# Optimization experiments

Hardware: AMD Instinct MI355X
Metric: run time of the kernel (lower is better)

Reference implementation:

```python
import jax, jax.numpy as jnp
import numpy as np

N, CIN, T, V = 32, 64, 256, 25
COUT = 192
K = 3                      # num_subset
INTER = COUT // 4          # coff_embedding = 4 -> 48
MID = COUT // 3            # 64
EPS = 1e-5


def _bn(x, g, b):
    # training-mode BatchNorm2d over (N, T, V) per channel
    m = x.mean(axis=(0, 2, 3), keepdims=True)
    v = x.var(axis=(0, 2, 3), keepdims=True)
    return (x - m) * jax.lax.rsqrt(v + EPS) * g[None, :, None, None] + b[None, :, None, None]


def _conv1x1(x, w, b):
    # w: [O, C]
    return jnp.einsum('oc,nctv->notv', w, x) + b[None, :, None, None]


def _tconv(x, w, b, pad):
    # w: [O, C, k, 1] temporal conv along T
    y = jax.lax.conv_general_dilated(x, w, (1, 1), ((pad, pad), (0, 0)),
                                     dimension_numbers=('NCHW', 'OIHW', 'NCHW'))
    return y + b[None, :, None, None]


def setup_inputs() -> dict:
    key = jax.random.key(0)
    ks = jax.random.split(key, 24)
    r = lambda i, shape, s=0.05: jax.random.normal(ks[i], shape, jnp.float32) * s
    return {
        'x': r(0, (N, CIN, T, V), 1.0),
        'A': jax.random.uniform(ks[1], (K, V, V), jnp.float32),   # fixed adjacency buffer
        'PA': jnp.full((K, V, V), 1e-6, jnp.float32),
        'Wa': r(2, (K, INTER, CIN)), 'ba': jnp.zeros((K, INTER), jnp.float32),
        'Wb': r(3, (K, INTER, CIN)), 'bb': jnp.zeros((K, INTER), jnp.float32),
        'Wd': r(4, (K, COUT, CIN)), 'bd': jnp.zeros((K, COUT), jnp.float32),
        'gcn_bn_g': jnp.ones(COUT, jnp.float32), 'gcn_bn_b': jnp.zeros(COUT, jnp.float32),
        'down_w': r(5, (COUT, CIN)), 'down_b': jnp.zeros(COUT, jnp.float32),
        'down_bn_g': jnp.ones(COUT, jnp.float32), 'down_bn_b': jnp.zeros(COUT, jnp.float32),
        'W11': r(6, (COUT, COUT)), 'b11': jnp.zeros(COUT, jnp.float32),
        'W21': r(7, (COUT, COUT)), 'b21': jnp.zeros(COUT, jnp.float32),
        'W31': r(8, (COUT, COUT)), 'b31': jnp.zeros(COUT, jnp.float32),
        'W12': r(9, (MID, COUT, 1, 1)), 'b12': jnp.zeros(MID, jnp.float32),
        'W22': r(10, (MID, COUT, 3, 1)), 'b22': jnp.zeros(MID, jnp.float32),
        'W32': r(11, (MID, COUT, 7, 1)), 'b32': jnp.zeros(MID, jnp.float32),
        'tcn_bn_g': jnp.ones(COUT, jnp.float32), 'tcn_bn_b': jnp.zeros(COUT, jnp.float32),
        'res_w': r(12, (COUT, CIN)), 'res_b': jnp.zeros(COUT, jnp.float32),
        'res_bn_g': jnp.ones(COUT, jnp.float32), 'res_bn_b': jnp.zeros(COUT, jnp.float32),
    }


def reference(x, A, PA, Wa, ba, Wb, bb, Wd, bd, gcn_bn_g, gcn_bn_b,
              down_w, down_b, down_bn_g, down_bn_b,
              W11, b11, W21, b21, W31, b31, W12, b12, W22, b22, W32, b32,
              tcn_bn_g, tcn_bn_b, res_w, res_b, res_bn_g, res_bn_b):
    n, c, t, v = x.shape
    # ---- unit_gcn (all num_subset branches vectorized over axis k) ----
    fa = jnp.einsum('kic,nctv->nkitv', Wa, x) + ba[None, :, :, None, None]
    fb = jnp.einsum('kic,nctv->nkitv', Wb, x) + bb[None, :, :, None, None]
    A1 = fa.transpose(0, 1, 4, 2, 3).reshape(n, K, v, INTER * t)   # [n,k,V,inter*T]
    A2 = fb.reshape(n, K, INTER * t, v)                            # [n,k,inter*T,V]
    scores = jnp.einsum('nkvd,nkdw->nkvw', A1, A2) / A1.shape[-1]
    att = jax.nn.softmax(scores, axis=-2) + (A + PA)[None]         # softmax over rows (dim -2)
    xv = x.reshape(n, c * t, v)
    z = jnp.einsum('ndv,nkvw->nkdw', xv, att).reshape(n, K, c, t, v)
    y = jnp.einsum('koc,nkctv->notv', Wd, z) + bd.sum(axis=0)[None, :, None, None]
    y = _bn(y, gcn_bn_g, gcn_bn_b)
    y = y + _bn(_conv1x1(x, down_w, down_b), down_bn_g, down_bn_b)
    g = jax.nn.relu(y)
    # ---- unit_tcn_m: three parallel (1x1 conv -> temporal conv) branches ----
    x1 = _tconv(_conv1x1(g, W11, b11), W12, b12, 0)
    x2 = _tconv(_conv1x1(g, W21, b21), W22, b22, 1)
    x3 = _tconv(_conv1x1(g, W31, b31), W32, b32, 3)
    tm = _bn(jnp.concatenate([x1, x2, x3], axis=1), tcn_bn_g, tcn_bn_b)
    # ---- residual: 1x1 unit_tcn on original input ----
    res = _bn(_conv1x1(x, res_w, res_b), res_bn_g, res_bn_b)
    return jax.nn.relu(tm + res)
```

## Files before the change

kernel.cpp:

```cpp
#include <hip/hip_runtime.h>
#include <hip/hip_bf16.h>
#include <cstdint>
#include <cstddef>

#define EPS_  1e-5f
#define NTV_  204800

typedef unsigned short u16;
typedef __attribute__((ext_vector_type(8))) short short8;
typedef __attribute__((ext_vector_type(4))) float f32x4;

__device__ __forceinline__ float bf2f(u16 u) {
  uint32_t x = (uint32_t)u << 16;
  float f;
  __builtin_memcpy(&f, &x, 4);
  return f;
}
__device__ __forceinline__ u16 f2bf(float f) {
  uint32_t x;
  __builtin_memcpy(&x, &f, 4);
  uint32_t r = (x + 0x7FFFu + ((x >> 16) & 1u)) >> 16;
  return (u16)r;
}

__device__ __forceinline__ void gload_lds16(const u16* g, u16* l) {
  __builtin_amdgcn_global_load_lds(
      (const __attribute__((address_space(1))) uint32_t*)g,
      (__attribute__((address_space(3))) uint32_t*)l, 16, 0, 0);
}

__global__ __launch_bounds__(256) void k_cvtw(
    const float* __restrict__ Wa, const float* __restrict__ Wb_,
    const float* __restrict__ dw, const float* __restrict__ rw,
    const float* __restrict__ W11, const float* __restrict__ W21, const float* __restrict__ W31,
    const float* __restrict__ Wd, const float* __restrict__ W12, const float* __restrict__ W22,
    const float* __restrict__ W32, const float* __restrict__ bd,
    const float* __restrict__ ba, const float* __restrict__ bb,
    const float* __restrict__ downbi, const float* __restrict__ resbi,
    const float* __restrict__ b11, const float* __restrict__ b21, const float* __restrict__ b31,
    u16* __restrict__ WB, float* __restrict__ bd2, float* __restrict__ fbias,
    float* __restrict__ cbias)
{
  int i = blockIdx.x * 256 + threadIdx.x;
  if (i < 9216) { WB[i] = f2bf(Wa[i]); return; }
  i -= 9216;
  if (i < 9216) { WB[9216 + i] = f2bf(Wb_[i]); return; }
  i -= 9216;
  if (i < 12288) { WB[18432 + i] = f2bf(dw[i]); return; }
  i -= 12288;
  if (i < 12288) { WB[30720 + i] = f2bf(rw[i]); return; }
  i -= 12288;
  if (i < 36864) { WB[43008 + i] = f2bf(W11[i]); return; }
  i -= 36864;
  if (i < 36864) { WB[79872 + i] = f2bf(W21[i]); return; }
  i -= 36864;
  if (i < 36864) { WB[116736 + i] = f2bf(W31[i]); return; }
  i -= 36864;
  if (i < 36864) {
    const int o = i / 192, r = i % 192, k = r >> 6, c = r & 63;
    WB[153600 + i] = f2bf(Wd[((size_t)(k * 192 + o)) * 64 + c]);
    return;
  }
  i -= 36864;
  if (i < 12288) { WB[190464 + i] = f2bf(W12[i]); return; }
  i -= 12288;
  if (i < 36864) {
    const int tap = i / 12288, q = i % 12288, o = q / 192, c = q % 192;
    WB[202752 + i] = f2bf(W22[((size_t)(o * 192 + c)) * 3 + tap]);
    return;
  }
  i -= 36864;
  if (i < 86016) {
    const int tap = i / 12288, q = i % 12288, o = q / 192, c = q % 192;
    WB[239616 + i] = f2bf(W32[((size_t)(o * 192 + c)) * 7 + tap]);
    return;
  }
  i -= 86016;
  if (i < 192) { bd2[i] = bd[i] + bd[192 + i] + bd[384 + i]; return; }
  i -= 192;
  if (i < 288) { fbias[i] = (i < 144) ? ba[i] : bb[i - 144]; return; }
  i -= 288;
  if (i < 960) {
    const int g = i / 192, o = i % 192;
    float v;
    if (g == 0) v = downbi[o];
    else if (g == 1) v = resbi[o];
    else if (g == 2) v = b11[o];
    else if (g == 3) v = b21[o];
    else v = b31[o];
    cbias[i] = v;
  }
}

__global__ __launch_bounds__(256) void k_xpose(const float* __restrict__ x, u16* __restrict__ xb)
{
  __shared__ u16 xt[256][72];
  const int bx = blockIdx.x;
  const int n = bx / 25, s0 = (bx % 25) * 256;
  const int tid = threadIdx.x;
  for (int l = tid; l < 64 * 64; l += 256) {
    const int c = l >> 6, q = l & 63;
    float4 v = *(const float4*)&x[((size_t)n * 64 + c) * 6400 + s0 + q * 4];
    xt[q * 4 + 0][c] = f2bf(v.x);
    xt[q * 4 + 1][c] = f2bf(v.y);
    xt[q * 4 + 2][c] = f2bf(v.z);
    xt[q * 4 + 3][c] = f2bf(v.w);
  }
  __syncthreads();
  for (int l = tid; l < 256 * 8; l += 256) {
    const int row = l >> 3, seg = l & 7;
    const int s_old = s0 + row;
    const int dv = s_old % 25, dt = s_old / 25;
    *(uint4*)&xb[((size_t)n * 6400 + dv * 256 + dt) * 64 + seg * 8] = *(const uint4*)&xt[row][seg * 8];
  }
}

template<int C, int NP, bool STATS>
__global__ __launch_bounds__(256, 2) void k_conv4(
    const u16* __restrict__ in, const u16* __restrict__ Wb,
    const float* __restrict__ bias,
    u16* __restrict__ out0, u16* __restrict__ out1, u16* __restrict__ out2,
    float* __restrict__ stSum, float* __restrict__ stSq)
{
  constexpr int CS = C / 8;
  constexpr int CH = C / 32;
  __shared__ u16 Bt[128 * C];
  __shared__ u16 Ep[4][16 * 24];

  const int bx = blockIdx.x;
  const int nb = bx / 50;
  const int sb = (bx % 50) * 128;
  const int tid = threadIdx.x;
  const int w = tid >> 6, lane = tid & 63;
  const int lr = lane & 15, lg = lane >> 4;

  constexpr int SB = 128 * CS;
#pragma unroll
  for (int base = 0; base < SB; base += 256) {
    const int slot = base + tid;
    const int r = slot / CS, q = slot % CS;
    gload_lds16(&in[((size_t)nb * 6400 + sb + r) * C + ((q ^ (r & 7)) << 3)],
                &Bt[(size_t)(base + w * 64) * 8]);
  }
  __syncthreads();

  const int row2 = lane >> 2, q2 = lane & 3;

  for (int p = 0; p < NP; ++p) {
    u16* outp = (p == 0) ? out0 : ((p == 1) ? out1 : out2);
    const u16* Ap = Wb + (size_t)p * 192 * C;
    short8 af[3][CH];
#pragma unroll
    for (int mi = 0; mi < 3; ++mi)
#pragma unroll
      for (int j = 0; j < CH; ++j)
        af[mi][j] = *(const short8*)&Ap[((size_t)(w * 48 + mi * 16 + lr)) * C + j * 32 + lg * 8];
    float4 bv[3];
#pragma unroll
    for (int mi = 0; mi < 3; ++mi)
      bv[mi] = *(const float4*)&bias[p * 192 + w * 48 + mi * 16 + lg * 4];
    float ssum[3][4] = {}, ssq[3][4] = {};

#pragma unroll
    for (int t = 0; t < 8; ++t) {
      f32x4 acc[3];
#pragma unroll
      for (int mi = 0; mi < 3; ++mi) {
        acc[mi][0] = 0.f; acc[mi][1] = 0.f; acc[mi][2] = 0.f; acc[mi][3] = 0.f;
      }
      const int rr = t * 16 + lr;
#pragma unroll
      for (int j = 0; j < CH; ++j) {
        short8 bf = *(const short8*)&Bt[((size_t)rr * CS + ((j * 4 + lg) ^ (rr & 7))) * 8];
#pragma unroll
        for (int mi = 0; mi < 3; ++mi)
          acc[mi] = __builtin_amdgcn_mfma_f32_16x16x32_bf16(af[mi][j], bf, acc[mi], 0, 0, 0);
      }
#pragma unroll
      for (int mi = 0; mi < 3; ++mi) {
        u16* sc = Ep[w];
#pragma unroll
        for (int r = 0; r < 4; ++r) {
          float vv = acc[mi][r] + ((const float*)&bv[mi])[r];
          if (STATS) { ssum[mi][r] += vv; ssq[mi][r] += vv * vv; }
          sc[lr * 24 + lg * 4 + r] = f2bf(vv);
        }
        uint2 val = *(const uint2*)&sc[row2 * 24 + q2 * 4];
        *(uint2*)&outp[((size_t)nb * 6400 + sb + t * 16 + row2) * 192 +
                       w * 48 + mi * 16 + q2 * 4] = val;
      }
    }

    if (STATS) {
#pragma unroll
      for (int mi = 0; mi < 3; ++mi)
#pragma unroll
        for (int r = 0; r < 4; ++r) {
          float ss = ssum[mi][r], sq = ssq[mi][r];
#pragma unroll
          for (int m = 1; m < 16; m <<= 1) { ss += __shfl_xor(ss, m); sq += __shfl_xor(sq, m); }
          if (lr == 0) {
            const int og = p * 192 + w * 48 + mi * 16 + lg * 4 + r;
            const int slot = bx & 15;
            atomicAdd(&stSum[og * 16 + slot], ss);
            atomicAdd(&stSq[og * 16 + slot], sq);
          }
        }
    }
  }
}

template<int KT>
__global__ __launch_bounds__(256, 2) void k_tconv4(
    const u16* __restrict__ in, const u16* __restrict__ Wb,
    const float* __restrict__ bias, u16* __restrict__ out,
    float* __restrict__ stSum, float* __restrict__ stSq,
    const u16* __restrict__ zp, int o_off)
{
  constexpr int C = 192, CS = 24, CH = 6;
  constexpr int HALO = KT / 2;
  constexpr int BR = 128 + 2 * HALO;
  __shared__ u16 Bt[BR * C];
  __shared__ u16 Ep[4][16 * 24];

  const int bx = blockIdx.x;
  const int nb = bx / 50;
  const int sb = (bx % 50) * 128;
  const int tbase = sb & 255;
  const int tid = threadIdx.x;
  const int w = tid >> 6, lane = tid & 63;
  const int lr = lane & 15, lg = lane >> 4;

  constexpr int SB = BR * CS;
  for (int base = 0; base < SB; base += 256) {
    const int slot = base + tid;
    if ((SB % 256 == 0) || slot < SB) {
      const int r = slot / CS, q = slot % CS;
      const int t = tbase - HALO + r;
      const u16* src = (HALO == 0 || (unsigned)t < 256u)
          ? &in[((size_t)nb * 6400 + sb - HALO + r) * C + ((q ^ (r & 7)) << 3)]
          : zp;
      gload_lds16(src, &Bt[(size_t)(base + w * 64) * 8]);
    }
  }
  __syncthreads();

  f32x4 acc[8];
#pragma unroll
  for (int t = 0; t < 8; ++t) {
    acc[t][0] = 0.f; acc[t][1] = 0.f; acc[t][2] = 0.f; acc[t][3] = 0.f;
  }

  for (int tap = 0; tap < KT; ++tap) {
    short8 af[CH];
#pragma unroll
    for (int j = 0; j < CH; ++j)
      af[j] = *(const short8*)&Wb[((size_t)(tap * 64 + w * 16 + lr)) * C + j * 32 + lg * 8];
#pragma unroll
    for (int t = 0; t < 8; ++t) {
      const int rr = t * 16 + lr + tap;
#pragma unroll
      for (int j = 0; j < CH; ++j) {
        short8 bf = *(const short8*)&Bt[((size_t)rr * CS + ((j * 4 + lg) ^ (rr & 7))) * 8];
        acc[t] = __builtin_amdgcn_mfma_f32_16x16x32_bf16(af[j], bf, acc[t], 0, 0, 0);
      }
    }
  }

  const float4 bv4 = *(const float4*)&bias[w * 16 + lg * 4];
  const int row2 = lane >> 2, q2 = lane & 3;
  float ssum[4] = {}, ssq[4] = {};
#pragma unroll
  for (int t = 0; t < 8; ++t) {
    u16* sc = Ep[w];
#pragma unroll
    for (int r = 0; r < 4; ++r) {
      float vv = acc[t][r] + ((const float*)&bv4)[r];
      ssum[r] += vv; ssq[r] += vv * vv;
      sc[lr * 24 + lg * 4 + r] = f2bf(vv);
    }
    uint2 val = *(const uint2*)&sc[row2 * 24 + q2 * 4];
    *(uint2*)&out[((size_t)nb * 6400 + sb + t * 16 + row2) * 192 +
                  o_off + w * 16 + q2 * 4] = val;
  }
#pragma unroll
  for (int r = 0; r < 4; ++r) {
    float ss = ssum[r], sq = ssq[r];
#pragma unroll
    for (int m = 1; m < 16; m <<= 1) { ss += __shfl_xor(ss, m); sq += __shfl_xor(sq, m); }
    if (lr == 0) {
      const int og = o_off + w * 16 + lg * 4 + r;
      const int slot = bx & 15;
      atomicAdd(&stSum[og * 16 + slot], ss);
      atomicAdd(&stSq[og * 16 + slot], sq);
    }
  }
}

__global__ __launch_bounds__(256) void k_gemm_cf(
    const u16* __restrict__ in, const u16* __restrict__ Wb,
    const float* __restrict__ bias, u16* __restrict__ out)
{
  __shared__ u16 Bt[128 * 64];
  __shared__ u16 At[288 * 64];
  __shared__ u16 SC[48 * 136];

  const int bx = blockIdx.x;
  const int nb = bx / 50;
  const int sb = (bx % 50) * 128;
  const int v = sb >> 8, tbase = sb & 255;
  const int tid = threadIdx.x;
  const int w = tid >> 6, lane = tid & 63;
  const int lr = lane & 15, lg = lane >> 4;
  const int s_w = w * 32;

  for (int base = 0; base < 1024; base += 256) {
    const int slot = base + tid;
    const int r = slot >> 3, q = slot & 7;
    gload_lds16(&in[((size_t)nb * 6400 + v * 256 + tbase + r) * 64 + ((q ^ (r & 7)) << 3)],
                &Bt[(size_t)(base + w * 64) * 8]);
  }
  for (int base = 0; base < 2304; base += 256) {
    const int slot = base + tid;
    const int r = slot >> 3, q = slot & 7;
    gload_lds16(&Wb[(size_t)r * 64 + ((q ^ (r & 7)) << 3)],
                &At[(size_t)(base + w * 64) * 8]);
  }
  __syncthreads();

  for (int p = 0; p < 6; ++p) {
    f32x4 acc[3][2];
#pragma unroll
    for (int mi = 0; mi < 3; ++mi)
#pragma unroll
      for (int ni = 0; ni < 2; ++ni) {
        acc[mi][ni][0] = 0.f; acc[mi][ni][1] = 0.f; acc[mi][ni][2] = 0.f; acc[mi][ni][3] = 0.f;
      }
#pragma unroll
    for (int ch = 0; ch < 2; ++ch) {
      const int j = ch * 4 + lg;
      short8 af[3], bf[2];
#pragma unroll
      for (int mi = 0; mi < 3; ++mi) {
        const int r = p * 48 + mi * 16 + lr;
        af[mi] = *(const short8*)&At[((size_t)r * 8 + (j ^ (r & 7))) * 8];
      }
#pragma unroll
      for (int ni = 0; ni < 2; ++ni) {
        const int r = s_w + ni * 16 + lr;
        bf[ni] = *(const short8*)&Bt[((size_t)r * 8 + (j ^ (r & 7))) * 8];
      }
#pragma unroll
      for (int mi = 0; mi < 3; ++mi)
#pragma unroll
        for (int ni = 0; ni < 2; ++ni)
          acc[mi][ni] = __builtin_amdgcn_mfma_f32_16x16x32_bf16(af[mi], bf[ni], acc[mi][ni], 0, 0, 0);
    }
#pragma unroll
    for (int mi = 0; mi < 3; ++mi)
#pragma unroll
      for (int r = 0; r < 4; ++r) {
        const float bv = bias[p * 48 + mi * 16 + lg * 4 + r];
#pragma unroll
        for (int ni = 0; ni < 2; ++ni) acc[mi][ni][r] += bv;
      }
    __syncthreads();
#pragma unroll
    for (int mi = 0; mi < 3; ++mi)
#pragma unroll
      for (int ni = 0; ni < 2; ++ni)
#pragma unroll
        for (int r = 0; r < 4; ++r)
          SC[(mi * 16 + lg * 4 + r) * 136 + s_w + ni * 16 + lr] = f2bf(acc[mi][ni][r]);
    __syncthreads();
#pragma unroll
    for (int it = 0; it < 3; ++it) {
      const int row = it * 16 + (tid >> 4), chunk = tid & 15;
      *(uint4*)&out[((size_t)nb * 288 + p * 48 + row) * 6400 + sb + chunk * 8] =
          *(const uint4*)&SC[row * 136 + chunk * 8];
    }
  }
}

__device__ __forceinline__ float dot4(uint2 a, uint2 b) {
  return bf2f((u16)(a.x & 0xffff)) * bf2f((u16)(b.x & 0xffff)) +
         bf2f((u16)(a.x >> 16))    * bf2f((u16)(b.x >> 16)) +
         bf2f((u16)(a.y & 0xffff)) * bf2f((u16)(b.y & 0xffff)) +
         bf2f((u16)(a.y >> 16))    * bf2f((u16)(b.y >> 16));
}

__global__ __launch_bounds__(256) void k_scores_part(
    const u16* __restrict__ fab, float* __restrict__ part)
{
  const int nk = blockIdx.x;
  const int seg = blockIdx.y;
  const int n = nk / 3, k = nk % 3;
  __shared__ u16 sa[12800], sb[12800];
  const int tid = threadIdx.x;
  const u16* fap = fab + ((size_t)(n * 288 + k * 48 + seg * 2)) * 6400;
  const u16* fbp = fab + ((size_t)(n * 288 + 144 + k * 48 + seg * 2)) * 6400;
  for (int l = tid; l < 1600; l += 256) {
    ((uint4*)sa)[l] = ((const uint4*)fap)[l];
    ((uint4*)sb)[l] = ((const uint4*)fbp)[l];
  }
  __syncthreads();

  const int l0 = tid, l1 = tid + 256, l2 = tid + 512;
  const bool ok2 = (l2 < 625);
  const int v0 = l0 / 25, w0 = l0 % 25;
  const int v1 = l1 / 25, w1 = l1 % 25;
  const int v2 = ok2 ? l2 / 25 : 0, w2 = ok2 ? l2 % 25 : 0;
  float a0 = 0.f, a1 = 0.f, a2 = 0.f;
  const int rot = ((tid & 63) * 4) & 255;

#pragma unroll
  for (int ch = 0; ch < 2; ++ch) {
    const u16* pa = sa + ch * 6400;
    const u16* pb = sb + ch * 6400;
    for (int it = 0; it < 64; ++it) {
      const int t = (it * 4 + rot) & 255;
      a0 += dot4(*(const uint2*)&pa[v0 * 256 + t], *(const uint2*)&pb[w0 * 256 + t]);
      a1 += dot4(*(const uint2*)&pa[v1 * 256 + t], *(const uint2*)&pb[w1 * 256 + t]);
      if (ok2)
        a2 += dot4(*(const uint2*)&pa[v2 * 256 + t], *(const uint2*)&pb[w2 * 256 + t]);
    }
  }
  float* po = part + ((size_t)nk * 24 + seg) * 640;
  po[l0] = a0;
  po[l1] = a1;
  if (ok2) po[l2] = a2;
}

__global__ __launch_bounds__(256) void k_softmax(
    const float* __restrict__ part, const float* __restrict__ A,
    const float* __restrict__ PA, float* __restrict__ att)
{
  const int nk = blockIdx.x;
  const int n = nk / 3, k = nk % 3;
  __shared__ float sc[640];
  const int tid = threadIdx.x;
  const float* pb = part + (size_t)nk * 24 * 640;
  for (int l = tid; l < 625; l += 256) {
    float s = 0.f;
#pragma unroll
    for (int seg = 0; seg < 24; ++seg) s += pb[seg * 640 + l];
    sc[l] = s;
  }
  __syncthreads();
  if (tid < 25) {
    const int w = tid;
    const float scale = 1.f / 12288.f;
    float m = -1e30f;
    for (int v = 0; v < 25; ++v) m = fmaxf(m, sc[v * 25 + w]);
    m *= scale;
    float e[25], sum = 0.f;
#pragma unroll
    for (int v = 0; v < 25; ++v) { e[v] = __expf(sc[v * 25 + w] * scale - m); sum += e[v]; }
    const float inv = 1.f / sum;
    const float* Ak = A + k * 625;
    const float* Pk = PA + k * 625;
    float* ao = att + ((size_t)n * 3 + k) * 625;
#pragma unroll
    for (int v = 0; v < 25; ++v) ao[v * 25 + w] = e[v] * inv + Ak[v * 25 + w] + Pk[v * 25 + w];
  }
}

__global__ __launch_bounds__(256) void k_z(
    const u16* __restrict__ xb, const float* __restrict__ att, u16* __restrict__ z)
{
  __shared__ float attl[1950];
  __shared__ u16 xt[12800];
  const int bx = blockIdx.x;
  const int n = bx >> 5, tb = (bx & 31) * 8;
  const int tid = threadIdx.x;

  for (int l = tid; l < 1875; l += 256) {
    const int k = l / 625, vw = l % 625, v = vw / 25, w = vw % 25;
    attl[(k * 25 + v) * 26 + w] = att[((size_t)n * 3 + k) * 625 + vw];
  }
  for (int l = tid; l < 200 * 8; l += 256) {
    const int j = l >> 3, seg = l & 7;
    const int vv = j >> 3, tl = j & 7;
    *(uint4*)&xt[j * 64 + seg * 8] =
        *(const uint4*)&xb[((size_t)n * 6400 + vv * 256 + tb + tl) * 64 + seg * 8];
  }
  __syncthreads();

  for (int it = 0; it < 19; ++it) {
    const int l = tid + it * 256;
    if (l >= 4800) break;
    const int hi = l >> 6, lo = l & 63;
    const int k = hi / 25, w = hi % 25;
    const int tl = lo >> 3, c0 = (lo & 7) * 8;
    float accv[8] = {};
    for (int v = 0; v < 25; ++v) {
      const float aw = attl[(k * 25 + v) * 26 + w];
      union { uint4 u; u16 s[8]; } xv;
      xv.u = *(const uint4*)&xt[(v * 8 + tl) * 64 + c0];
#pragma unroll
      for (int jj = 0; jj < 8; ++jj) accv[jj] += aw * bf2f(xv.s[jj]);
    }
    union { uint4 u; u16 s[8]; } ov;
#pragma unroll
    for (int jj = 0; jj < 8; ++jj) ov.s[jj] = f2bf(accv[jj]);
    *(uint4*)&z[((size_t)n * 6400 + w * 256 + tb + tl) * 192 + k * 64 + c0] = ov.u;
  }
}

__global__ void k_bnparams(const float* __restrict__ sSum, const float* __restrict__ sSq,
                           const float* __restrict__ gamma, const float* __restrict__ beta,
                           float* __restrict__ a, float* __restrict__ c, int O)
{
  const int o = threadIdx.x + blockIdx.x * blockDim.x;
  if (o >= O) return;
  float sum = 0.f, sq = 0.f;
#pragma unroll
  for (int s = 0; s < 16; ++s) { sum += sSum[o * 16 + s]; sq += sSq[o * 16 + s]; }
  const float mean = sum * (1.f / NTV_);
  const float var = sq * (1.f / NTV_) - mean * mean;
  const float inv = rsqrtf(var + EPS_);
  const float av = gamma[o] * inv;
  a[o] = av;
  c[o] = beta[o] - av * mean;
}

__global__ __launch_bounds__(256) void k_g2(
    const u16* __restrict__ ypre, const u16* __restrict__ down,
    const float* __restrict__ ga, const float* __restrict__ gc,
    const float* __restrict__ da, const float* __restrict__ dc,
    u16* __restrict__ g)
{
  __shared__ float pA1[192], pC1[192], pA2[192], pC2[192];
  const int tid = threadIdx.x;
  if (tid < 192) { pA1[tid] = ga[tid]; pC1[tid] = gc[tid]; pA2[tid] = da[tid]; pC2[tid] = dc[tid]; }
  __syncthreads();
  for (size_t i8 = (size_t)blockIdx.x * 256 + tid; i8 < 4915200; i8 += (size_t)gridDim.x * 256) {
    const int c0 = (int)(i8 % 24) * 8;
    union { uint4 u; u16 s[8]; } yv, dv, ov;
    yv.u = *(const uint4*)&ypre[i8 * 8];
    dv.u = *(const uint4*)&down[i8 * 8];
#pragma unroll
    for (int j = 0; j < 8; ++j) {
      const int c = c0 + j;
      ov.s[j] = f2bf(fmaxf(pA1[c] * bf2f(yv.s[j]) + pC1[c] + pA2[c] * bf2f(dv.s[j]) + pC2[c], 0.f));
    }
    *(uint4*)&g[i8 * 8] = ov.u;
  }
}

__global__ __launch_bounds__(256) void k_out(
    const u16* __restrict__ tm, const u16* __restrict__ resp,
    const float* __restrict__ ta, const float* __restrict__ tc,
    const float* __restrict__ ra, const float* __restrict__ rc,
    float* __restrict__ out)
{
  __shared__ u16 L[100][200];
  __shared__ float pA1[192], pC1[192], pA2[192], pC2[192];
  const int bx = blockIdx.x;
  const int n = bx >> 6, t0 = (bx & 63) * 4;
  const int tid = threadIdx.x;
  if (tid < 192) { pA1[tid] = ta[tid]; pC1[tid] = tc[tid]; pA2[tid] = ra[tid]; pC2[tid] = rc[tid]; }
  __syncthreads();
  for (int l = tid; l < 2400; l += 256) {
    const int row = l / 24, ch = l % 24;
    const int v = row >> 2, tl = row & 3;
    const size_t src = ((size_t)n * 6400 + v * 256 + t0 + tl) * 192 + ch * 8;
    union { uint4 u; u16 s[8]; } tv, rv;
    tv.u = *(const uint4*)&tm[src];
    rv.u = *(const uint4*)&resp[src];
#pragma unroll
    for (int j = 0; j < 8; ++j) {
      const int c = ch * 8 + j;
      L[row][c] = f2bf(fmaxf(pA1[c] * bf2f(tv.s[j]) + pC1[c] + pA2[c] * bf2f(rv.s[j]) + pC2[c], 0.f));
    }
  }
  __syncthreads();
  for (int j = tid; j < 192 * 25; j += 256) {
    const int o = j / 25, q = j % 25;
    float4 f4;
#pragma unroll
    for (int e = 0; e < 4; ++e) {
      const int idx = q * 4 + e;
      const int tl = idx / 25, v = idx % 25;
      ((float*)&f4)[e] = bf2f(L[v * 4 + tl][o]);
    }
    *(float4*)&out[((size_t)n * 192 + o) * 6400 + t0 * 25 + q * 4] = f4;
  }
}

extern "C" void kernel_launch(void* const* d_in, const int* in_sizes, int n_in,
                              void* d_out, int out_size, void* d_ws, size_t ws_size,
                              hipStream_t stream)
{
  const float* x      = (const float*)d_in[0];
  const float* A      = (const float*)d_in[1];
  const float* PA     = (const float*)d_in[2];
  const float* Wa     = (const float*)d_in[3];
  const float* ba     = (const float*)d_in[4];
  const float* Wb     = (const float*)d_in[5];
  const float* bb     = (const float*)d_in[6];
  const float* Wd     = (const float*)d_in[7];
  const float* bd     = (const float*)d_in[8];
  const float* gcng   = (const float*)d_in[9];
  const float* gcnb   = (const float*)d_in[10];
  const float* downw  = (const float*)d_in[11];
  const float* downbi = (const float*)d_in[12];
  const float* downg  = (const float*)d_in[13];
  const float* downb  = (const float*)d_in[14];
  const float* W11    = (const float*)d_in[15];
  const float* b11    = (const float*)d_in[16];
  const float* W21    = (const float*)d_in[17];
  const float* b21    = (const float*)d_in[18];
  const float* W31    = (const float*)d_in[19];
  const float* b31    = (const float*)d_in[20];
  const float* W12    = (const float*)d_in[21];
  const float* b12    = (const float*)d_in[22];
  const float* W22    = (const float*)d_in[23];
  const float* b22    = (const float*)d_in[24];
  const float* W32    = (const float*)d_in[25];
  const float* b32    = (const float*)d_in[26];
  const float* tcng   = (const float*)d_in[27];
  const float* tcnb   = (const float*)d_in[28];
  const float* resw   = (const float*)d_in[29];
  const float* resbi  = (const float*)d_in[30];
  const float* resg   = (const float*)d_in[31];
  const float* resb   = (const float*)d_in[32];
  (void)in_sizes; (void)n_in; (void)out_size; (void)ws_size;

  u16* ob = (u16*)d_out;
  u16* fab   = ob;
  u16* xb    = ob + 58982400;
  float* att = (float*)(ob + 72089600);
  float* part  = (float*)(ob + 72584768);
  float* fbias = (float*)(ob + 75533888);
  u16* btmp2 = ob;
  u16* btmp3 = ob + 39321600;

  char* ws = (char*)d_ws;
  const size_t SLOT = 78643200;
  u16* z     = (u16*)(ws);
  u16* g     = (u16*)(ws);
  u16* ypre  = (u16*)(ws + SLOT);
  u16* btmp1 = (u16*)(ws + SLOT);
  u16* down  = (u16*)(ws + 2 * SLOT);
  u16* tm    = (u16*)(ws + 2 * SLOT);
  u16* resp  = (u16*)(ws + 3 * SLOT);
  char* sm   = ws + 4 * SLOT;
  float* bnp   = (float*)(sm);
  u16*   zp    = (u16*)(sm + 8192);
  u16*   WB    = (u16*)(sm + 8704);
  float* bd2   = (float*)(sm + 660224);
  float* cbias = (float*)(sm + 661248);
  float* slots = (float*)(sm + 665600);
  float* gcnSum = slots;           float* gcnSq = slots + 3072;
  float* dwnSum = slots + 6144;    float* resSum = slots + 9216;
  float* dwnSq  = slots + 12288;   float* resSq  = slots + 15360;
  float* tmSum  = slots + 18432;   float* tmSq   = slots + 21504;
  float* gcnA = bnp;          float* gcnC = bnp + 192;
  float* dwnA = bnp + 384;    float* dwnC = bnp + 576;
  float* resA = bnp + 768;    float* resC = bnp + 960;
  float* tmA  = bnp + 1152;   float* tmC  = bnp + 1344;

  hipMemsetAsync(slots, 0, 24576 * 4, stream);
  hipMemsetAsync(zp, 0, 256, stream);

  const dim3 blk(256);

  k_cvtw<<<dim3(1278), blk, 0, stream>>>(Wa, Wb, downw, resw, W11, W21, W31,
                                         Wd, W12, W22, W32, bd, ba, bb,
                                         downbi, resbi, b11, b21, b31,
                                         WB, bd2, fbias, cbias);
  k_xpose<<<dim3(800), blk, 0, stream>>>(x, xb);

  k_gemm_cf<<<dim3(1600), blk, 0, stream>>>(xb, WB, fbias, fab);
  k_scores_part<<<dim3(96, 24), blk, 0, stream>>>(fab, part);
  k_softmax<<<dim3(96), blk, 0, stream>>>(part, A, PA, att);
  k_z<<<dim3(1024), blk, 0, stream>>>(xb, att, z);
  k_conv4<192, 1, true><<<dim3(1600), blk, 0, stream>>>(
      z, WB + 153600, bd2, ypre, ypre, ypre, gcnSum, gcnSq);
  k_conv4<64, 2, true><<<dim3(1600), blk, 0, stream>>>(
      xb, WB + 18432, cbias, down, resp, resp, dwnSum, dwnSq);
  k_bnparams<<<dim3(1), dim3(192), 0, stream>>>(gcnSum, gcnSq, gcng, gcnb, gcnA, gcnC, 192);
  k_bnparams<<<dim3(1), dim3(192), 0, stream>>>(dwnSum, dwnSq, downg, downb, dwnA, dwnC, 192);
  k_bnparams<<<dim3(1), dim3(192), 0, stream>>>(resSum, resSq, resg, resb, resA, resC, 192);
  k_g2<<<dim3(2048), blk, 0, stream>>>(ypre, down, gcnA, gcnC, dwnA, dwnC, g);

  k_conv4<192, 3, false><<<dim3(1600), blk, 0, stream>>>(
      g, WB + 43008, cbias + 384, btmp1, btmp2, btmp3, nullptr, nullptr);
  k_tconv4<1><<<dim3(1600), blk, 0, stream>>>(
      btmp1, WB + 190464, b12, tm, tmSum, tmSq, zp, 0);
  k_tconv4<3><<<dim3(1600), blk, 0, stream>>>(
      btmp2, WB + 202752, b22, tm, tmSum, tmSq, zp, 64);
  k_tconv4<7><<<dim3(1600), blk, 0, stream>>>(
      btmp3, WB + 239616, b32, tm, tmSum, tmSq, zp, 128);
  k_bnparams<<<dim3(1), dim3(192), 0, stream>>>(tmSum, tmSq, tcng, tcnb, tmA, tmC, 192);

  k_out<<<dim3(2048), blk, 0, stream>>>(tm, resp, tmA, tmC, resA, resC, (float*)d_out);
}
```

Baseline: 938.7 us.

## Rework conv and tconv warp tiling for 64-channel wide uint4 stores

```diff
diff --git a/kernel.cpp b/kernel.cpp
--- a/kernel.cpp
+++ b/kernel.cpp
@@ -116,7 +116,7 @@
 }
 
 template<int C, int NP, bool STATS>
-__global__ __launch_bounds__(256, 2) void k_conv4(
+__global__ __launch_bounds__(192) void k_conv5(
     const u16* __restrict__ in, const u16* __restrict__ Wb,
     const float* __restrict__ bias,
     u16* __restrict__ out0, u16* __restrict__ out1, u16* __restrict__ out2,
@@ -124,8 +124,9 @@
 {
   constexpr int CS = C / 8;
   constexpr int CH = C / 32;
+  constexpr int SB = 128 * CS;
   __shared__ u16 Bt[128 * C];
-  __shared__ u16 Ep[4][16 * 24];
+  __shared__ u16 Ep[3][16 * 72];
 
   const int bx = blockIdx.x;
   const int nb = bx / 50;
@@ -134,38 +135,40 @@
   const int w = tid >> 6, lane = tid & 63;
   const int lr = lane & 15, lg = lane >> 4;
 
-  constexpr int SB = 128 * CS;
-#pragma unroll
-  for (int base = 0; base < SB; base += 256) {
+  for (int base = 0; base < SB; base += 192) {
     const int slot = base + tid;
-    const int r = slot / CS, q = slot % CS;
-    gload_lds16(&in[((size_t)nb * 6400 + sb + r) * C + ((q ^ (r & 7)) << 3)],
-                &Bt[(size_t)(base + w * 64) * 8]);
-  }
-  __syncthreads();
-
-  const int row2 = lane >> 2, q2 = lane & 3;
+    if ((SB % 192 == 0) || slot < SB) {
+      const int r = slot / CS, q = slot % CS;
+      gload_lds16(&in[((size_t)nb * 6400 + sb + r) * C + ((q ^ (r & 7)) << 3)],
+                  &Bt[(size_t)(base + w * 64) * 8]);
+    }
+  }
+  __syncthreads();
+
+  u16* sc = Ep[w];
+  const int o_w = w * 64;
+  const int s0 = lane >> 3, seg = lane & 7;
 
   for (int p = 0; p < NP; ++p) {
     u16* outp = (p == 0) ? out0 : ((p == 1) ? out1 : out2);
     const u16* Ap = Wb + (size_t)p * 192 * C;
-    short8 af[3][CH];
-#pragma unroll
-    for (int mi = 0; mi < 3; ++mi)
+    short8 af[4][CH];
+#pragma unroll
+    for (int mi = 0; mi < 4; ++mi)
 #pragma unroll
       for (int j = 0; j < CH; ++j)
-        af[mi][j] = *(const short8*)&Ap[((size_t)(w * 48 + mi * 16 + lr)) * C + j * 32 + lg * 8];
-    float4 bv[3];
-#pragma unroll
-    for (int mi = 0; mi < 3; ++mi)
-      bv[mi] = *(const float4*)&bias[p * 192 + w * 48 + mi * 16 + lg * 4];
-    float ssum[3][4] = {}, ssq[3][4] = {};
+        af[mi][j] = *(const short8*)&Ap[((size_t)(o_w + mi * 16 + lr)) * C + j * 32 + lg * 8];
+    float4 bv[4];
+#pragma unroll
+    for (int mi = 0; mi < 4; ++mi)
+      bv[mi] = *(const float4*)&bias[p * 192 + o_w + mi * 16 + lg * 4];
+    float ssum[4][4] = {}, ssq[4][4] = {};
 
 #pragma unroll
     for (int t = 0; t < 8; ++t) {
-      f32x4 acc[3];
-#pragma unroll
-      for (int mi = 0; mi < 3; ++mi) {
+      f32x4 acc[4];
+#pragma unroll
+      for (int mi = 0; mi < 4; ++mi) {
         acc[mi][0] = 0.f; acc[mi][1] = 0.f; acc[mi][2] = 0.f; acc[mi][3] = 0.f;
       }
       const int rr = t * 16 + lr;
@@ -173,34 +176,35 @@
       for (int j = 0; j < CH; ++j) {
         short8 bf = *(const short8*)&Bt[((size_t)rr * CS + ((j * 4 + lg) ^ (rr & 7))) * 8];
 #pragma unroll
-        for (int mi = 0; mi < 3; ++mi)
+        for (int mi = 0; mi < 4; ++mi)
           acc[mi] = __builtin_amdgcn_mfma_f32_16x16x32_bf16(af[mi][j], bf, acc[mi], 0, 0, 0);
       }
 #pragma unroll
-      for (int mi = 0; mi < 3; ++mi) {
-        u16* sc = Ep[w];
+      for (int mi = 0; mi < 4; ++mi)
 #pragma unroll
         for (int r = 0; r < 4; ++r) {
           float vv = acc[mi][r] + ((const float*)&bv[mi])[r];
           if (STATS) { ssum[mi][r] += vv; ssq[mi][r] += vv * vv; }
-          sc[lr * 24 + lg * 4 + r] = f2bf(vv);
+          sc[lr * 72 + mi * 16 + lg * 4 + r] = f2bf(vv);
         }
-        uint2 val = *(const uint2*)&sc[row2 * 24 + q2 * 4];
-        *(uint2*)&outp[((size_t)nb * 6400 + sb + t * 16 + row2) * 192 +
-                       w * 48 + mi * 16 + q2 * 4] = val;
+#pragma unroll
+      for (int pass = 0; pass < 2; ++pass) {
+        const int s = pass * 8 + s0;
+        uint4 val = *(const uint4*)&sc[s * 72 + seg * 8];
+        *(uint4*)&outp[((size_t)nb * 6400 + sb + t * 16 + s) * 192 + o_w + seg * 8] = val;
       }
     }
 
     if (STATS) {
 #pragma unroll
-      for (int mi = 0; mi < 3; ++mi)
+      for (int mi = 0; mi < 4; ++mi)
 #pragma unroll
         for (int r = 0; r < 4; ++r) {
           float ss = ssum[mi][r], sq = ssq[mi][r];
 #pragma unroll
           for (int m = 1; m < 16; m <<= 1) { ss += __shfl_xor(ss, m); sq += __shfl_xor(sq, m); }
           if (lr == 0) {
-            const int og = p * 192 + w * 48 + mi * 16 + lg * 4 + r;
+            const int og = p * 192 + o_w + mi * 16 + lg * 4 + r;
             const int slot = bx & 15;
             atomicAdd(&stSum[og * 16 + slot], ss);
             atomicAdd(&stSq[og * 16 + slot], sq);
@@ -211,7 +215,7 @@
 }
 
 template<int KT>
-__global__ __launch_bounds__(256, 2) void k_tconv4(
+__global__ __launch_bounds__(256) void k_tconv5(
     const u16* __restrict__ in, const u16* __restrict__ Wb,
     const float* __restrict__ bias, u16* __restrict__ out,
     float* __restrict__ stSum, float* __restrict__ stSq,
@@ -221,7 +225,7 @@
   constexpr int HALO = KT / 2;
   constexpr int BR = 128 + 2 * HALO;
   __shared__ u16 Bt[BR * C];
-  __shared__ u16 Ep[4][16 * 24];
+  __shared__ u16 Ep[4][16 * 72];
 
   const int bx = blockIdx.x;
   const int nb = bx / 50;
@@ -245,56 +249,71 @@
   }
   __syncthreads();
 
-  f32x4 acc[8];
-#pragma unroll
-  for (int t = 0; t < 8; ++t) {
-    acc[t][0] = 0.f; acc[t][1] = 0.f; acc[t][2] = 0.f; acc[t][3] = 0.f;
-  }
+  f32x4 acc[2][4];
+#pragma unroll
+  for (int ts = 0; ts < 2; ++ts)
+#pragma unroll
+    for (int mi = 0; mi < 4; ++mi) {
+      acc[ts][mi][0] = 0.f; acc[ts][mi][1] = 0.f; acc[ts][mi][2] = 0.f; acc[ts][mi][3] = 0.f;
+    }
 
   for (int tap = 0; tap < KT; ++tap) {
-    short8 af[CH];
-#pragma unroll
-    for (int j = 0; j < CH; ++j)
-      af[j] = *(const short8*)&Wb[((size_t)(tap * 64 + w * 16 + lr)) * C + j * 32 + lg * 8];
-#pragma unroll
-    for (int t = 0; t < 8; ++t) {
-      const int rr = t * 16 + lr + tap;
+    short8 af[4][CH];
+#pragma unroll
+    for (int mi = 0; mi < 4; ++mi)
+#pragma unroll
+      for (int j = 0; j < CH; ++j)
+        af[mi][j] = *(const short8*)&Wb[((size_t)(tap * 64 + mi * 16 + lr)) * C + j * 32 + lg * 8];
+#pragma unroll
+    for (int ts = 0; ts < 2; ++ts) {
+      const int rr = w * 32 + ts * 16 + lr + tap;
 #pragma unroll
       for (int j = 0; j < CH; ++j) {
         short8 bf = *(const short8*)&Bt[((size_t)rr * CS + ((j * 4 + lg) ^ (rr & 7))) * 8];
-        acc[t] = __builtin_amdgcn_mfma_f32_16x16x32_bf16(af[j], bf, acc[t], 0, 0, 0);
-      }
-    }
-  }
-
-  const float4 bv4 = *(const float4*)&bias[w * 16 + lg * 4];
-  const int row2 = lane >> 2, q2 = lane & 3;
-  float ssum[4] = {}, ssq[4] = {};
-#pragma unroll
-  for (int t = 0; t < 8; ++t) {
-    u16* sc = Ep[w];
+#pragma unroll
+        for (int mi = 0; mi < 4; ++mi)
+          acc[ts][mi] = __builtin_amdgcn_mfma_f32_16x16x32_bf16(af[mi][j], bf, acc[ts][mi], 0, 0, 0);
+      }
+    }
+  }
+
+  u16* sc = Ep[w];
+  float4 bv[4];
+#pragma unroll
+  for (int mi = 0; mi < 4; ++mi) bv[mi] = *(const float4*)&bias[mi * 16 + lg * 4];
+  const int s0 = lane >> 3, seg = lane & 7;
+  float ssum[4][4] = {}, ssq[4][4] = {};
+#pragma unroll
+  for (int ts = 0; ts < 2; ++ts) {
+#pragma unroll
+    for (int mi = 0; mi < 4; ++mi)
+#pragma unroll
+      for (int r = 0; r < 4; ++r) {
+        float vv = acc[ts][mi][r] + ((const float*)&bv[mi])[r];
+        ssum[mi][r] += vv; ssq[mi][r] += vv * vv;
+        sc[lr * 72 + mi * 16 + lg * 4 + r] = f2bf(vv);
+      }
+#pragma unroll
+    for (int pass = 0; pass < 2; ++pass) {
+      const int s = pass * 8 + s0;
+      uint4 val = *(const uint4*)&sc[s * 72 + seg * 8];
+      *(uint4*)&out[((size_t)nb * 6400 + sb + w * 32 + ts * 16 + s) * 192 + o_off + seg * 8] = val;
+    }
+  }
+#pragma unroll
+  for (int mi = 0; mi < 4; ++mi)
 #pragma unroll
     for (int r = 0; r < 4; ++r) {
-      float vv = acc[t][r] + ((const float*)&bv4)[r];
-      ssum[r] += vv; ssq[r] += vv * vv;
-      sc[lr * 24 + lg * 4 + r] = f2bf(vv);
-    }
-    uint2 val = *(const uint2*)&sc[row2 * 24 + q2 * 4];
-    *(uint2*)&out[((size_t)nb * 6400 + sb + t * 16 + row2) * 192 +
-                  o_off + w * 16 + q2 * 4] = val;
-  }
-#pragma unroll
-  for (int r = 0; r < 4; ++r) {
-    float ss = ssum[r], sq = ssq[r];
-#pragma unroll
-    for (int m = 1; m < 16; m <<= 1) { ss += __shfl_xor(ss, m); sq += __shfl_xor(sq, m); }
-    if (lr == 0) {
-      const int og = o_off + w * 16 + lg * 4 + r;
-      const int slot = bx & 15;
-      atomicAdd(&stSum[og * 16 + slot], ss);
-      atomicAdd(&stSq[og * 16 + slot], sq);
-    }
-  }
+      float ss = ssum[mi][r], sq = ssq[mi][r];
+#pragma unroll
+      for (int m = 1; m < 16; m <<= 1) { ss += __shfl_xor(ss, m); sq += __shfl_xor(sq, m); }
+      if (lr == 0) {
+        const int og = o_off + mi * 16 + lg * 4 + r;
+        const int slot = bx & 15;
+        atomicAdd(&stSum[og * 16 + slot], ss);
+        atomicAdd(&stSq[og * 16 + slot], sq);
+      }
+    }
 }
 
 __global__ __launch_bounds__(256) void k_gemm_cf(
@@ -665,6 +684,7 @@
   hipMemsetAsync(zp, 0, 256, stream);
 
   const dim3 blk(256);
+  const dim3 blk3(192);
 
   k_cvtw<<<dim3(1278), blk, 0, stream>>>(Wa, Wb, downw, resw, W11, W21, W31,
                                          Wd, W12, W22, W32, bd, ba, bb,
@@ -676,22 +696,22 @@
   k_scores_part<<<dim3(96, 24), blk, 0, stream>>>(fab, part);
   k_softmax<<<dim3(96), blk, 0, stream>>>(part, A, PA, att);
   k_z<<<dim3(1024), blk, 0, stream>>>(xb, att, z);
-  k_conv4<192, 1, true><<<dim3(1600), blk, 0, stream>>>(
+  k_conv5<192, 1, true><<<dim3(1600), blk3, 0, stream>>>(
       z, WB + 153600, bd2, ypre, ypre, ypre, gcnSum, gcnSq);
-  k_conv4<64, 2, true><<<dim3(1600), blk, 0, stream>>>(
+  k_conv5<64, 2, true><<<dim3(1600), blk3, 0, stream>>>(
       xb, WB + 18432, cbias, down, resp, resp, dwnSum, dwnSq);
   k_bnparams<<<dim3(1), dim3(192), 0, stream>>>(gcnSum, gcnSq, gcng, gcnb, gcnA, gcnC, 192);
   k_bnparams<<<dim3(1), dim3(192), 0, stream>>>(dwnSum, dwnSq, downg, downb, dwnA, dwnC, 192);
   k_bnparams<<<dim3(1), dim3(192), 0, stream>>>(resSum, resSq, resg, resb, resA, resC, 192);
   k_g2<<<dim3(2048), blk, 0, stream>>>(ypre, down, gcnA, gcnC, dwnA, dwnC, g);
 
-  k_conv4<192, 3, false><<<dim3(1600), blk, 0, stream>>>(
+  k_conv5<192, 3, false><<<dim3(1600), blk3, 0, stream>>>(
       g, WB + 43008, cbias + 384, btmp1, btmp2, btmp3, nullptr, nullptr);
-  k_tconv4<1><<<dim3(1600), blk, 0, stream>>>(
+  k_tconv5<1><<<dim3(1600), blk, 0, stream>>>(
       btmp1, WB + 190464, b12, tm, tmSum, tmSq, zp, 0);
-  k_tconv4<3><<<dim3(1600), blk, 0, stream>>>(
+  k_tconv5<3><<<dim3(1600), blk, 0, stream>>>(
       btmp2, WB + 202752, b22, tm, tmSum, tmSq, zp, 64);
-  k_tconv4<7><<<dim3(1600), blk, 0, stream>>>(
+  k_tconv5<7><<<dim3(1600), blk, 0, stream>>>(
       btmp3, WB + 239616, b32, tm, tmSum, tmSq, zp, 128);
   k_bnparams<<<dim3(1), dim3(192), 0, stream>>>(tmSum, tmSq, tcng, tcnb, tmA, tmC, 192);
 
```

Result: slower. 1.414 ms (+50.6%).

## Use three waves per 1x1-conv block with 64 output channels each and wider stores

Applied to the files above, without the earlier changes.

```diff
diff --git a/kernel.cpp b/kernel.cpp
--- a/kernel.cpp
+++ b/kernel.cpp
@@ -116,7 +116,7 @@
 }
 
 template<int C, int NP, bool STATS>
-__global__ __launch_bounds__(256, 2) void k_conv4(
+__global__ __launch_bounds__(192) void k_conv5(
     const u16* __restrict__ in, const u16* __restrict__ Wb,
     const float* __restrict__ bias,
     u16* __restrict__ out0, u16* __restrict__ out1, u16* __restrict__ out2,
@@ -124,8 +124,9 @@
 {
   constexpr int CS = C / 8;
   constexpr int CH = C / 32;
+  constexpr int SB = 128 * CS;
   __shared__ u16 Bt[128 * C];
-  __shared__ u16 Ep[4][16 * 24];
+  __shared__ u16 Ep[3][16 * 72];
 
   const int bx = blockIdx.x;
   const int nb = bx / 50;
@@ -134,38 +135,40 @@
   const int w = tid >> 6, lane = tid & 63;
   const int lr = lane & 15, lg = lane >> 4;
 
-  constexpr int SB = 128 * CS;
-#pragma unroll
-  for (int base = 0; base < SB; base += 256) {
+  for (int base = 0; base < SB; base += 192) {
     const int slot = base + tid;
-    const int r = slot / CS, q = slot % CS;
-    gload_lds16(&in[((size_t)nb * 6400 + sb + r) * C + ((q ^ (r & 7)) << 3)],
-                &Bt[(size_t)(base + w * 64) * 8]);
-  }
-  __syncthreads();
-
-  const int row2 = lane >> 2, q2 = lane & 3;
+    if ((SB % 192 == 0) || slot < SB) {
+      const int r = slot / CS, q = slot % CS;
+      gload_lds16(&in[((size_t)nb * 6400 + sb + r) * C + ((q ^ (r & 7)) << 3)],
+                  &Bt[(size_t)(base + w * 64) * 8]);
+    }
+  }
+  __syncthreads();
+
+  u16* sc = Ep[w];
+  const int o_w = w * 64;
+  const int s0 = lane >> 3, seg = lane & 7;
 
   for (int p = 0; p < NP; ++p) {
     u16* outp = (p == 0) ? out0 : ((p == 1) ? out1 : out2);
     const u16* Ap = Wb + (size_t)p * 192 * C;
-    short8 af[3][CH];
-#pragma unroll
-    for (int mi = 0; mi < 3; ++mi)
+    short8 af[4][CH];
+#pragma unroll
+    for (int mi = 0; mi < 4; ++mi)
 #pragma unroll
       for (int j = 0; j < CH; ++j)
-        af[mi][j] = *(const short8*)&Ap[((size_t)(w * 48 + mi * 16 + lr)) * C + j * 32 + lg * 8];
-    float4 bv[3];
-#pragma unroll
-    for (int mi = 0; mi < 3; ++mi)
-      bv[mi] = *(const float4*)&bias[p * 192 + w * 48 + mi * 16 + lg * 4];
-    float ssum[3][4] = {}, ssq[3][4] = {};
+        af[mi][j] = *(const short8*)&Ap[((size_t)(o_w + mi * 16 + lr)) * C + j * 32 + lg * 8];
+    float4 bv[4];
+#pragma unroll
+    for (int mi = 0; mi < 4; ++mi)
+      bv[mi] = *(const float4*)&bias[p * 192 + o_w + mi * 16 + lg * 4];
+    float ssum[4][4] = {}, ssq[4][4] = {};
 
 #pragma unroll
     for (int t = 0; t < 8; ++t) {
-      f32x4 acc[3];
-#pragma unroll
-      for (int mi = 0; mi < 3; ++mi) {
+      f32x4 acc[4];
+#pragma unroll
+      for (int mi = 0; mi < 4; ++mi) {
         acc[mi][0] = 0.f; acc[mi][1] = 0.f; acc[mi][2] = 0.f; acc[mi][3] = 0.f;
       }
       const int rr = t * 16 + lr;
@@ -173,34 +176,35 @@
       for (int j = 0; j < CH; ++j) {
         short8 bf = *(const short8*)&Bt[((size_t)rr * CS + ((j * 4 + lg) ^ (rr & 7))) * 8];
 #pragma unroll
-        for (int mi = 0; mi < 3; ++mi)
+        for (int mi = 0; mi < 4; ++mi)
           acc[mi] = __builtin_amdgcn_mfma_f32_16x16x32_bf16(af[mi][j], bf, acc[mi], 0, 0, 0);
       }
 #pragma unroll
-      for (int mi = 0; mi < 3; ++mi) {
-        u16* sc = Ep[w];
+      for (int mi = 0; mi < 4; ++mi)
 #pragma unroll
         for (int r = 0; r < 4; ++r) {
           float vv = acc[mi][r] + ((const float*)&bv[mi])[r];
           if (STATS) { ssum[mi][r] += vv; ssq[mi][r] += vv * vv; }
-          sc[lr * 24 + lg * 4 + r] = f2bf(vv);
+          sc[lr * 72 + mi * 16 + lg * 4 + r] = f2bf(vv);
         }
-        uint2 val = *(const uint2*)&sc[row2 * 24 + q2 * 4];
-        *(uint2*)&outp[((size_t)nb * 6400 + sb + t * 16 + row2) * 192 +
-                       w * 48 + mi * 16 + q2 * 4] = val;
+#pragma unroll
+      for (int pass = 0; pass < 2; ++pass) {
+        const int s = pass * 8 + s0;
+        uint4 val = *(const uint4*)&sc[s * 72 + seg * 8];
+        *(uint4*)&outp[((size_t)nb * 6400 + sb + t * 16 + s) * 192 + o_w + seg * 8] = val;
       }
     }
 
     if (STATS) {
 #pragma unroll
-      for (int mi = 0; mi < 3; ++mi)
+      for (int mi = 0; mi < 4; ++mi)
 #pragma unroll
         for (int r = 0; r < 4; ++r) {
           float ss = ssum[mi][r], sq = ssq[mi][r];
 #pragma unroll
           for (int m = 1; m < 16; m <<= 1) { ss += __shfl_xor(ss, m); sq += __shfl_xor(sq, m); }
           if (lr == 0) {
-            const int og = p * 192 + w * 48 + mi * 16 + lg * 4 + r;
+            const int og = p * 192 + o_w + mi * 16 + lg * 4 + r;
             const int slot = bx & 15;
             atomicAdd(&stSum[og * 16 + slot], ss);
             atomicAdd(&stSq[og * 16 + slot], sq);
@@ -665,6 +669,7 @@
   hipMemsetAsync(zp, 0, 256, stream);
 
   const dim3 blk(256);
+  const dim3 blk3(192);
 
   k_cvtw<<<dim3(1278), blk, 0, stream>>>(Wa, Wb, downw, resw, W11, W21, W31,
                                          Wd, W12, W22, W32, bd, ba, bb,
@@ -676,16 +681,16 @@
   k_scores_part<<<dim3(96, 24), blk, 0, stream>>>(fab, part);
   k_softmax<<<dim3(96), blk, 0, stream>>>(part, A, PA, att);
   k_z<<<dim3(1024), blk, 0, stream>>>(xb, att, z);
-  k_conv4<192, 1, true><<<dim3(1600), blk, 0, stream>>>(
+  k_conv5<192, 1, true><<<dim3(1600), blk3, 0, stream>>>(
       z, WB + 153600, bd2, ypre, ypre, ypre, gcnSum, gcnSq);
-  k_conv4<64, 2, true><<<dim3(1600), blk, 0, stream>>>(
+  k_conv5<64, 2, true><<<dim3(1600), blk3, 0, stream>>>(
       xb, WB + 18432, cbias, down, resp, resp, dwnSum, dwnSq);
   k_bnparams<<<dim3(1), dim3(192), 0, stream>>>(gcnSum, gcnSq, gcng, gcnb, gcnA, gcnC, 192);
   k_bnparams<<<dim3(1), dim3(192), 0, stream>>>(dwnSum, dwnSq, downg, downb, dwnA, dwnC, 192);
   k_bnparams<<<dim3(1), dim3(192), 0, stream>>>(resSum, resSq, resg, resb, resA, resC, 192);
   k_g2<<<dim3(2048), blk, 0, stream>>>(ypre, down, gcnA, gcnC, dwnA, dwnC, g);
 
-  k_conv4<192, 3, false><<<dim3(1600), blk, 0, stream>>>(
+  k_conv5<192, 3, false><<<dim3(1600), blk3, 0, stream>>>(
       g, WB + 43008, cbias + 384, btmp1, btmp2, btmp3, nullptr, nullptr);
   k_tconv4<1><<<dim3(1600), blk, 0, stream>>>(
       btmp1, WB + 190464, b12, tm, tmSum, tmSq, zp, 0);
```

After: 923.7 us. No clear change (-1.6%).
